# Performance work log

Measured on AMD Instinct MI355X. Metric: run time of the kernel, lower is better.

## Reference

```python
import jax, jax.numpy as jnp
import numpy as np

B, NPG, H, D = 16, 4096, 2, 64            # graphs, nodes/graph, heads, in_channels
N = B * NPG                                # 65536 total nodes
E_PER = 32768                              # edges per graph (avg degree 8)
E = B * E_PER                              # 524288 total edges
K_ORDER = 4
BETA = 0.5
D_OUT = 64


def setup_inputs():
    key = jax.random.key(0)
    k = jax.random.split(key, 10)
    x = jax.random.normal(k[0], (N, D), jnp.float32)
    # intra-graph random edges (block-diagonal adjacency)
    src = jax.random.randint(k[1], (B, E_PER), 0, NPG)
    dst = jax.random.randint(k[2], (B, E_PER), 0, NPG)
    off = (jnp.arange(B) * NPG)[:, None]
    edge_index = jnp.stack([(src + off).reshape(-1), (dst + off).reshape(-1)], axis=0)
    batch = jnp.arange(N) // NPG
    s = 1.0 / np.sqrt(D)
    Wq = jax.random.normal(k[3], (D, D * H), jnp.float32) * s
    bq = jnp.zeros((D * H,), jnp.float32)
    Wk = jax.random.normal(k[4], (D, D * H), jnp.float32) * s
    bk = jnp.zeros((D * H,), jnp.float32)
    Wo = jax.random.normal(k[5], (D * H, D_OUT), jnp.float32) * (1.0 / np.sqrt(D * H))
    bo = jnp.zeros((D_OUT,), jnp.float32)
    return {"x": x, "edge_index": edge_index, "batch": batch,
            "Wq": Wq, "bq": bq, "Wk": Wk, "bk": bk, "Wo": Wo, "bo": bo}


def reference(x, edge_index, batch, Wq, bq, Wk, bk, Wo, bo):
    Nn = x.shape[0]
    q = (x @ Wq + bq).reshape(Nn, H, D)
    k = (x @ Wk + bk).reshape(Nn, H, D)
    qs = q / jnp.linalg.norm(q, axis=2, keepdims=True)
    ks = k / jnp.linalg.norm(k, axis=2, keepdims=True)

    # symmetric-normalized transposed adjacency: adj_t[col_e, row_e] = w_e
    row, col = edge_index[0], edge_index[1]
    w = jnp.ones((row.shape[0],), x.dtype)
    deg = jax.ops.segment_sum(w, col, num_segments=N)
    dinv = jnp.where(deg > 0, deg ** -0.5, 0.0)
    val = dinv[col] * w * dinv[row]

    def gcn(xs):  # xs [N,H,D]; out[i] = sum_{e: col_e==i} val_e * xs[row_e]
        return jax.ops.segment_sum(val[:, None, None] * xs[row], col, num_segments=N)

    # ragged block <-> padded batch conversion (block-sorted batch ids)
    counts = jax.ops.segment_sum(jnp.ones((Nn,), jnp.int32), batch, num_segments=B)
    starts = jnp.concatenate([jnp.zeros((1,), jnp.int32), jnp.cumsum(counts)[:-1]])
    pos = jnp.arange(Nn) - starts[batch]

    def to_batch(v):
        return jnp.zeros((B, NPG) + v.shape[1:], v.dtype).at[batch, pos].set(v)

    def to_block(v):
        return v[batch, pos]

    qs_b, ks_b = to_batch(qs), to_batch(ks)      # [B, NPG, H, D]
    xs = jnp.broadcast_to(x[:, None, :], (Nn, H, D))
    xs_b = to_batch(xs)

    # linear (kernelized) attention; note source adds B (=qs.shape[0]) to the
    # denominator and uses the pre-loop xs_batch for every iteration -- kept faithful.
    kvs = jnp.einsum('blhm,blhd->bhmd', ks_b, xs_b)
    qkvs = jnp.einsum('bnhm,bhmd->bnhd', qs_b, kvs)
    num = qkvs + xs_b.sum(axis=1)[:, None]                       # [B,NPG,H,D]
    den = jnp.einsum('bnhm,bhm->bnh', qs_b, ks_b.sum(axis=1))[..., None] + float(B)
    attn_blk = to_block(num / den)                               # [N,H,D]

    for _ in range(K_ORDER):
        xs = xs + BETA * gcn(xs) + (1.0 - BETA) * attn_blk

    return (xs.reshape(Nn, H * D) @ Wo + bo) / H
```

## Files before the change

### kernel.cpp

```cpp
#include <hip/hip_runtime.h>

#define N_NODES 65536
#define B_G     16
#define NPG_    4096
#define H_H     2
#define D_D     64
#define HD      128
#define E_E     524288
#define D_OUT   64


__global__ void deg_kernel(const int* __restrict__ col, int* __restrict__ degi) {
    int e = blockIdx.x * 256 + threadIdx.x;
    if (e < E_E) atomicAdd(&degi[col[e]], 1);
}

__global__ void scan1(const int* __restrict__ degi, int* __restrict__ ptr,
                      int* __restrict__ bsums, float* __restrict__ dinv) {
    __shared__ int lds[256];
    int t = threadIdx.x;
    int i = blockIdx.x * 256 + t;
    int v = degi[i];
    dinv[i] = (v > 0) ? (1.0f / sqrtf((float)v)) : 0.0f;
    lds[t] = v;
    __syncthreads();
    for (int off = 1; off < 256; off <<= 1) {
        int tmp = (t >= off) ? lds[t - off] : 0;
        __syncthreads();
        lds[t] += tmp;
        __syncthreads();
    }
    ptr[i] = lds[t] - v;
    if (t == 255) bsums[blockIdx.x] = lds[255];
}

__global__ void scan3(int* __restrict__ ptr, const int* __restrict__ bsums) {
    __shared__ int red[256];
    int t = threadIdx.x;
    red[t] = (t < (int)blockIdx.x) ? bsums[t] : 0;
    __syncthreads();
    for (int off = 128; off > 0; off >>= 1) {
        if (t < off) red[t] += red[t + off];
        __syncthreads();
    }
    int i = blockIdx.x * 256 + t;
    ptr[i] += red[0];
    if (i == 0) ptr[N_NODES] = E_E;
}

__global__ void scatter_kernel(const int* __restrict__ row, const int* __restrict__ col,
                               const int* __restrict__ ptr, int* __restrict__ cursor,
                               const float* __restrict__ dinv,
                               int2* __restrict__ ep) {
    int e = blockIdx.x * 256 + threadIdx.x;
    if (e < E_E) {
        int c = col[e], r = row[e];
        int p = ptr[c] + atomicAdd(&cursor[c], 1);
        ep[p] = make_int2(r, __float_as_int(dinv[c] * dinv[r]));
    }
}

__global__ __launch_bounds__(256) void proj_kernel(
    const float* __restrict__ x,
    const float* __restrict__ Wq, const float* __restrict__ bq,
    const float* __restrict__ Wk, const float* __restrict__ bk,
    float* __restrict__ qs, float* __restrict__ ks) {
    __shared__ float4 wt4[16 * 128];
    __shared__ float4 xt4[64 * 17];
    __shared__ float bl[128];
    int t = threadIdx.x;
    int qk = blockIdx.x & 1;
    int nb = (blockIdx.x >> 1) * 64;
    const float* W = qk ? Wk : Wq;
    const float* bias = qk ? bk : bq;
    float* outp = qk ? ks : qs;

    for (int i = t; i < 2048; i += 256) {
        int k4 = i >> 7, c = i & 127;
        wt4[i] = make_float4(W[(4 * k4 + 0) * 128 + c], W[(4 * k4 + 1) * 128 + c],
                             W[(4 * k4 + 2) * 128 + c], W[(4 * k4 + 3) * 128 + c]);
    }
    const float4* xg = (const float4*)(x + (size_t)nb * 64);
    for (int i = t; i < 1024; i += 256) {
        int node = i >> 4, k4 = i & 15;
        xt4[node * 17 + k4] = xg[i];
    }
    if (t < 128) bl[t] = bias[t];
    __syncthreads();

    int cg = t & 15;
    int nd = (t >> 4) & 3;
    int w = t >> 6;
    int n_t = w * 16 + nd * 4;

    float acc[4][8];
#pragma unroll
    for (int i = 0; i < 4; ++i)
#pragma unroll
        for (int j = 0; j < 8; ++j) acc[i][j] = 0.f;

#pragma unroll 2
    for (int k4 = 0; k4 < 16; ++k4) {
        float4 xv0 = xt4[(n_t + 0) * 17 + k4];
        float4 xv1 = xt4[(n_t + 1) * 17 + k4];
        float4 xv2 = xt4[(n_t + 2) * 17 + k4];
        float4 xv3 = xt4[(n_t + 3) * 17 + k4];
#pragma unroll
        for (int j = 0; j < 8; ++j) {
            float4 wv = wt4[k4 * 128 + cg + 16 * j];
            acc[0][j] += wv.x * xv0.x + wv.y * xv0.y + wv.z * xv0.z + wv.w * xv0.w;
            acc[1][j] += wv.x * xv1.x + wv.y * xv1.y + wv.z * xv1.z + wv.w * xv1.w;
            acc[2][j] += wv.x * xv2.x + wv.y * xv2.y + wv.z * xv2.z + wv.w * xv2.w;
            acc[3][j] += wv.x * xv3.x + wv.y * xv3.y + wv.z * xv3.z + wv.w * xv3.w;
        }
    }

    float bcol[8];
#pragma unroll
    for (int j = 0; j < 8; ++j) bcol[j] = bl[cg + 16 * j];

#pragma unroll
    for (int i = 0; i < 4; ++i) {
#pragma unroll
        for (int j = 0; j < 8; ++j) acc[i][j] += bcol[j];
        float s0 = acc[i][0] * acc[i][0] + acc[i][1] * acc[i][1] +
                   acc[i][2] * acc[i][2] + acc[i][3] * acc[i][3];
        float s1 = acc[i][4] * acc[i][4] + acc[i][5] * acc[i][5] +
                   acc[i][6] * acc[i][6] + acc[i][7] * acc[i][7];
#pragma unroll
        for (int off = 8; off > 0; off >>= 1) {
            s0 += __shfl_xor(s0, off);
            s1 += __shfl_xor(s1, off);
        }
        float r0 = rsqrtf(s0), r1 = rsqrtf(s1);
        size_t base = (size_t)(nb + n_t + i) * 128 + cg;
#pragma unroll
        for (int j = 0; j < 4; ++j) outp[base + 16 * j] = acc[i][j] * r0;
#pragma unroll
        for (int j = 4; j < 8; ++j) outp[base + 16 * j] = acc[i][j] * r1;
    }
}

__global__ __launch_bounds__(256) void kvs_part(
    const float* __restrict__ ks, const float* __restrict__ x,
    float* __restrict__ partials, float* __restrict__ ksum, float* __restrict__ xsum) {
    int bid = blockIdx.x;
    int chunk = bid & 31;
    int bh = bid >> 5;
    int b = bh >> 1, h = bh & 1;
    int t = threadIdx.x;
    int mrow = t >> 4, dcol = t & 15;
    int m0 = mrow * 4, d0 = dcol * 4;
    __shared__ float kl[32 * 64];
    __shared__ float xl[32 * 64];
    float acc[4][4] = {{0}};
    float ksacc[4] = {0, 0, 0, 0};
    float xsacc[4] = {0, 0, 0, 0};
    int node0 = b * NPG_ + chunk * 128;
    for (int s = 0; s < 4; ++s) {
        int nb = node0 + s * 32;
        for (int i = t; i < 512; i += 256) {
            int l = i >> 4, q = i & 15;
            ((float4*)kl)[i] = *(const float4*)(ks + (size_t)(nb + l) * 128 + h * 64 + q * 4);
        }
        const float4* xg = (const float4*)(x + (size_t)nb * 64);
        for (int i = t; i < 512; i += 256) ((float4*)xl)[i] = xg[i];
        __syncthreads();
        for (int l = 0; l < 32; ++l) {
            float4 kv = *(float4*)(kl + l * 64 + m0);
            float4 xv = *(float4*)(xl + l * 64 + d0);
            float kk[4] = {kv.x, kv.y, kv.z, kv.w};
            float xx[4] = {xv.x, xv.y, xv.z, xv.w};
#pragma unroll
            for (int i = 0; i < 4; ++i)
#pragma unroll
                for (int j = 0; j < 4; ++j) acc[i][j] += kk[i] * xx[j];
            if (dcol == 0) {
#pragma unroll
                for (int i = 0; i < 4; ++i) ksacc[i] += kk[i];
            }
            if (mrow == 0) {
#pragma unroll
                for (int j = 0; j < 4; ++j) xsacc[j] += xx[j];
            }
        }
        __syncthreads();
    }
    float* pout = partials + (size_t)bid * 4096;
#pragma unroll
    for (int i = 0; i < 4; ++i)
        *(float4*)(pout + (m0 + i) * 64 + d0) =
            make_float4(acc[i][0], acc[i][1], acc[i][2], acc[i][3]);
    if (dcol == 0) {
#pragma unroll
        for (int i = 0; i < 4; ++i) atomicAdd(&ksum[bh * 64 + m0 + i], ksacc[i]);
    }
    if (mrow == 0 && h == 0) {
#pragma unroll
        for (int j = 0; j < 4; ++j) atomicAdd(&xsum[b * 64 + d0 + j], xsacc[j]);
    }
}

__global__ __launch_bounds__(256) void kvs_reduce(
    const float* __restrict__ partials, float* __restrict__ kvs) {
    int i = blockIdx.x * 256 + threadIdx.x;
    int bh = i >> 12, elem = i & 4095;
    const float* p = partials + (size_t)bh * 32 * 4096 + elem;
    float s = 0.f;
#pragma unroll
    for (int c = 0; c < 32; ++c) s += p[c * 4096];
    kvs[i] = s;
}

__global__ __launch_bounds__(256) void attn_kernel(
    const float* __restrict__ qs, const float* __restrict__ kvs,
    const float* __restrict__ ksum, const float* __restrict__ xsum,
    float* __restrict__ attn) {
    __shared__ float ql[128 * 64];
    int bid = blockIdx.x;
    int h = bid & 1;
    int nb = (bid >> 1) * 128;
    int b = nb >> 12;
    int bh = b * 2 + h;
    int t = threadIdx.x;
    int lane = t & 63;
    for (int i = t; i < 128 * 16; i += 256) {
        int r = i >> 4, q4 = i & 15;
        ((float4*)ql)[i] = *(const float4*)(qs + (size_t)(nb + r) * 128 + h * 64 + q4 * 4);
    }
    float kvreg[64];
    const float* kvp = kvs + bh * 4096 + lane;
#pragma unroll
    for (int m = 0; m < 64; ++m) kvreg[m] = kvp[m * 64];
    float ksreg = ksum[bh * 64 + lane];
    float xs_d = xsum[b * 64 + lane];
    __syncthreads();
    int nslot = t >> 6;
    for (int nn = 0; nn < 32; ++nn) {
        int node = nn * 4 + nslot;
        const float* qrow = ql + node * 64;
        float p = qrow[lane] * ksreg;
#pragma unroll
        for (int off = 32; off > 0; off >>= 1) p += __shfl_xor(p, off);
        float den = p + 16.0f;
        float acc = 0.f;
#pragma unroll
        for (int m4 = 0; m4 < 16; ++m4) {
            float4 qv = *(const float4*)(qrow + m4 * 4);
            acc += qv.x * kvreg[4 * m4] + qv.y * kvreg[4 * m4 + 1] +
                   qv.z * kvreg[4 * m4 + 2] + qv.w * kvreg[4 * m4 + 3];
        }
        attn[(size_t)(nb + node) * 128 + h * 64 + lane] = (acc + xs_d) / den;
    }
}

__global__ __launch_bounds__(256) void awo_kernel(
    const float* __restrict__ attn, const float* __restrict__ Wo,
    float* __restrict__ a) {
    __shared__ float4 wt4[32 * 64];
    __shared__ float4 xt4[64 * 32];
    int t = threadIdx.x;
    int nb = blockIdx.x * 64;

    for (int i = t; i < 2048; i += 256) {
        int k4 = i >> 6, c = i & 63;
        wt4[i] = make_float4(Wo[(4 * k4 + 0) * 64 + c], Wo[(4 * k4 + 1) * 64 + c],
                             Wo[(4 * k4 + 2) * 64 + c], Wo[(4 * k4 + 3) * 64 + c]);
    }
    const float4* ag = (const float4*)(attn + (size_t)nb * 128);
    for (int i = t; i < 2048; i += 256) xt4[i] = ag[i];
    __syncthreads();

    int cg = t & 15;
    int ns = t >> 4;
    int s = ns & 3;
    int n_t = ns * 4;

    float acc[4][4] = {{0.f}};
#pragma unroll 4
    for (int k4 = 0; k4 < 32; ++k4) {
        int kk = k4 ^ s;
        float4 xv0 = xt4[(n_t + 0) * 32 + kk];
        float4 xv1 = xt4[(n_t + 1) * 32 + kk];
        float4 xv2 = xt4[(n_t + 2) * 32 + kk];
        float4 xv3 = xt4[(n_t + 3) * 32 + kk];
#pragma unroll
        for (int j = 0; j < 4; ++j) {
            float4 wv = wt4[kk * 64 + cg + 16 * j];
            acc[0][j] += wv.x * xv0.x + wv.y * xv0.y + wv.z * xv0.z + wv.w * xv0.w;
            acc[1][j] += wv.x * xv1.x + wv.y * xv1.y + wv.z * xv1.z + wv.w * xv1.w;
            acc[2][j] += wv.x * xv2.x + wv.y * xv2.y + wv.z * xv2.z + wv.w * xv2.w;
            acc[3][j] += wv.x * xv3.x + wv.y * xv3.y + wv.z * xv3.z + wv.w * xv3.w;
        }
    }
#pragma unroll
    for (int i = 0; i < 4; ++i)
#pragma unroll
        for (int j = 0; j < 4; ++j)
            a[(size_t)(nb + n_t + i) * 64 + cg + 16 * j] = acc[i][j];
}

__global__ __launch_bounds__(256) void y0_kernel(
    const float* __restrict__ x, const float* __restrict__ Wo,
    float* __restrict__ y0) {
    __shared__ float4 wt4[16 * 64];
    __shared__ float4 xt4[64 * 16];
    int t = threadIdx.x;
    int nb = blockIdx.x * 64;

    for (int i = t; i < 1024; i += 256) {
        int k4 = i >> 6, c = i & 63;
        wt4[i] = make_float4(
            Wo[(4 * k4 + 0) * 64 + c] + Wo[(4 * k4 + 64) * 64 + c],
            Wo[(4 * k4 + 1) * 64 + c] + Wo[(4 * k4 + 65) * 64 + c],
            Wo[(4 * k4 + 2) * 64 + c] + Wo[(4 * k4 + 66) * 64 + c],
            Wo[(4 * k4 + 3) * 64 + c] + Wo[(4 * k4 + 67) * 64 + c]);
    }
    const float4* xg = (const float4*)(x + (size_t)nb * 64);
    for (int i = t; i < 1024; i += 256) xt4[i] = xg[i];
    __syncthreads();

    int cg = t & 15;
    int ns = t >> 4;
    int s = ns & 3;
    int n_t = ns * 4;

    float acc[4][4] = {{0.f}};
#pragma unroll 4
    for (int k4 = 0; k4 < 16; ++k4) {
        int kk = k4 ^ s;
        float4 xv0 = xt4[(n_t + 0) * 16 + kk];
        float4 xv1 = xt4[(n_t + 1) * 16 + kk];
        float4 xv2 = xt4[(n_t + 2) * 16 + kk];
        float4 xv3 = xt4[(n_t + 3) * 16 + kk];
#pragma unroll
        for (int j = 0; j < 4; ++j) {
            float4 wv = wt4[kk * 64 + cg + 16 * j];
            acc[0][j] += wv.x * xv0.x + wv.y * xv0.y + wv.z * xv0.z + wv.w * xv0.w;
            acc[1][j] += wv.x * xv1.x + wv.y * xv1.y + wv.z * xv1.z + wv.w * xv1.w;
            acc[2][j] += wv.x * xv2.x + wv.y * xv2.y + wv.z * xv2.z + wv.w * xv2.w;
            acc[3][j] += wv.x * xv3.x + wv.y * xv3.y + wv.z * xv3.z + wv.w * xv3.w;
        }
    }
#pragma unroll
    for (int i = 0; i < 4; ++i)
#pragma unroll
        for (int j = 0; j < 4; ++j)
            y0[(size_t)(nb + n_t + i) * 64 + cg + 16 * j] = acc[i][j];
}

template <int LAST>
__global__ __launch_bounds__(256) void gcn64_kernel(
    const float* __restrict__ yin, const float* __restrict__ a,
    const int* __restrict__ ptr, const int2* __restrict__ ep,
    float* __restrict__ yout, const float* __restrict__ bo) {
    int bid = blockIdx.x;
    int lbid = (bid & 7) * (N_NODES / 16 / 8) + (bid >> 3);
    int t = threadIdx.x;
    int n = lbid * 16 + (t >> 4);
    int lg = t & 15;
    int c4 = lg * 4;
    int e0 = ptr[n], e1 = ptr[n + 1];
    int cnt = e1 - e0;
    float4 acc = make_float4(0.f, 0.f, 0.f, 0.f);

    {
        int2 q[8];
#pragma unroll
        for (int i = 0; i < 8; ++i) {
            int ee = e0 + i;
            if (ee > e1 - 1) ee = e1 - 1;
            if (ee < 0) ee = 0;
            q[i] = ep[ee];
        }
#pragma unroll
        for (int i = 0; i < 8; ++i) {
            if (i < cnt) {
                float v = __int_as_float(q[i].y);
                float4 xv = *(const float4*)(yin + (size_t)q[i].x * 64 + c4);
                acc.x += v * xv.x; acc.y += v * xv.y;
                acc.z += v * xv.z; acc.w += v * xv.w;
            }
        }
    }
    if (cnt > 8) {
        int2 q[8];
#pragma unroll
        for (int i = 0; i < 8; ++i) {
            int ee = e0 + 8 + i;
            if (ee > e1 - 1) ee = e1 - 1;
            q[i] = ep[ee];
        }
#pragma unroll
        for (int i = 0; i < 8; ++i) {
            if (8 + i < cnt) {
                float v = __int_as_float(q[i].y);
                float4 xv = *(const float4*)(yin + (size_t)q[i].x * 64 + c4);
                acc.x += v * xv.x; acc.y += v * xv.y;
                acc.z += v * xv.z; acc.w += v * xv.w;
            }
        }
        for (int e = e0 + 16; e < e1; ++e) {
            int2 qq = ep[e];
            float v = __int_as_float(qq.y);
            float4 xv = *(const float4*)(yin + (size_t)qq.x * 64 + c4);
            acc.x += v * xv.x; acc.y += v * xv.y;
            acc.z += v * xv.z; acc.w += v * xv.w;
        }
    }

    size_t idx = (size_t)n * 64 + c4;
    float4 self = *(const float4*)(yin + idx);
    float4 at = *(const float4*)(a + idx);
    float4 o;
    o.x = self.x + 0.5f * acc.x + 0.5f * at.x;
    o.y = self.y + 0.5f * acc.y + 0.5f * at.y;
    o.z = self.z + 0.5f * acc.z + 0.5f * at.z;
    o.w = self.w + 0.5f * acc.w + 0.5f * at.w;
    if (LAST) {
        float4 bv = *(const float4*)(bo + c4);
        o.x = (o.x + bv.x) * 0.5f;
        o.y = (o.y + bv.y) * 0.5f;
        o.z = (o.z + bv.z) * 0.5f;
        o.w = (o.w + bv.w) * 0.5f;
    }
    *(float4*)(yout + idx) = o;
}


extern "C" void kernel_launch(void* const* d_in, const int* in_sizes, int n_in,
                              void* d_out, int out_size, void* d_ws, size_t ws_size,
                              hipStream_t stream) {
    const float* x  = (const float*)d_in[0];
    const int* ei   = (const int*)d_in[1];
    const float* Wq = (const float*)d_in[3];
    const float* bq = (const float*)d_in[4];
    const float* Wk = (const float*)d_in[5];
    const float* bk = (const float*)d_in[6];
    const float* Wo = (const float*)d_in[7];
    const float* bo = (const float*)d_in[8];
    float* out = (float*)d_out;

    const int* row = ei;
    const int* col = ei + E_E;

    float* bufA = (float*)d_ws;
    float* bufB = bufA + (size_t)N_NODES * HD;
    float* bufC = bufB + (size_t)N_NODES * HD;
    int2*  ep   = (int2*)(bufC + (size_t)N_NODES * HD);
    float* kvs  = (float*)(ep + E_E);
    float* ksum = kvs + 131072;
    float* xsum = ksum + 2048;
    float* dinv = xsum + 1024;
    int* degi   = (int*)(dinv + N_NODES);
    int* cursor = degi + N_NODES;
    int* ptr    = cursor + N_NODES;
    int* bsums  = ptr + N_NODES + 1;

    float* a_  = bufA;
    float* yA  = bufA + (size_t)N_NODES * 64;
    float* yB  = bufB;

    hipMemsetAsync(degi, 0, (size_t)N_NODES * 2 * 4, stream);
    hipMemsetAsync(ksum, 0, (size_t)(2048 + 1024) * 4, stream);

    deg_kernel<<<E_E / 256, 256, 0, stream>>>(col, degi);
    scan1<<<N_NODES / 256, 256, 0, stream>>>(degi, ptr, bsums, dinv);
    scan3<<<N_NODES / 256, 256, 0, stream>>>(ptr, bsums);
    scatter_kernel<<<E_E / 256, 256, 0, stream>>>(row, col, ptr, cursor, dinv, ep);

    proj_kernel<<<2048, 256, 0, stream>>>(x, Wq, bq, Wk, bk, bufA, bufB);

    kvs_part<<<1024, 256, 0, stream>>>(bufB, x, bufC, ksum, xsum);
    kvs_reduce<<<512, 256, 0, stream>>>(bufC, kvs);
    attn_kernel<<<1024, 256, 0, stream>>>(bufA, kvs, ksum, xsum, bufC);

    awo_kernel<<<1024, 256, 0, stream>>>(bufC, Wo, a_);
    y0_kernel<<<1024, 256, 0, stream>>>(x, Wo, yA);

    gcn64_kernel<0><<<N_NODES / 16, 256, 0, stream>>>(yA, a_, ptr, ep, yB, bo);
    gcn64_kernel<0><<<N_NODES / 16, 256, 0, stream>>>(yB, a_, ptr, ep, yA, bo);
    gcn64_kernel<0><<<N_NODES / 16, 256, 0, stream>>>(yA, a_, ptr, ep, yB, bo);
    gcn64_kernel<1><<<N_NODES / 16, 256, 0, stream>>>(yB, a_, ptr, ep, out, bo);
}
```

Measured before the change: 357.6 us.

## Retile projection and attention as register-blocked GEMMs, flatten GCN edge prefetch

The projection kernel now handles 128 nodes per block with an 8x8 register tile and XOR-swizzled shared memory in place of padding. The grid is halved to match. The attention kernel is rewritten from a per-lane 64-register kvs dot product into a tiled GEMM that stages kvs transposed in shared memory and computes the denominator inside the same loop. The GCN kernel unconditionally prefetches 16 edge entries instead of two conditional batches of 8. These changes aim for more register reuse and fewer bank conflicts, at the cost of more registers per thread and more redundant edge loads for low-degree nodes.

```diff
diff --git a/kernel.cpp b/kernel.cpp
--- a/kernel.cpp
+++ b/kernel.cpp
@@ -60,17 +60,16 @@
     }
 }
 
-__global__ __launch_bounds__(256) void proj_kernel(
+__global__ __launch_bounds__(256, 2) void proj_kernel(
     const float* __restrict__ x,
     const float* __restrict__ Wq, const float* __restrict__ bq,
     const float* __restrict__ Wk, const float* __restrict__ bk,
     float* __restrict__ qs, float* __restrict__ ks) {
     __shared__ float4 wt4[16 * 128];
-    __shared__ float4 xt4[64 * 17];
-    __shared__ float bl[128];
+    __shared__ float4 xt4[128 * 16];
     int t = threadIdx.x;
     int qk = blockIdx.x & 1;
-    int nb = (blockIdx.x >> 1) * 64;
+    int nb = (blockIdx.x >> 1) * 128;
     const float* W = qk ? Wk : Wq;
     const float* bias = qk ? bk : bq;
     float* outp = qk ? ks : qs;
@@ -81,46 +80,43 @@
                              W[(4 * k4 + 2) * 128 + c], W[(4 * k4 + 3) * 128 + c]);
     }
     const float4* xg = (const float4*)(x + (size_t)nb * 64);
-    for (int i = t; i < 1024; i += 256) {
+    for (int i = t; i < 2048; i += 256) {
         int node = i >> 4, k4 = i & 15;
-        xt4[node * 17 + k4] = xg[i];
-    }
-    if (t < 128) bl[t] = bias[t];
+        xt4[node * 16 + (k4 ^ (node & 7))] = xg[i];
+    }
     __syncthreads();
 
     int cg = t & 15;
-    int nd = (t >> 4) & 3;
-    int w = t >> 6;
-    int n_t = w * 16 + nd * 4;
-
-    float acc[4][8];
-#pragma unroll
-    for (int i = 0; i < 4; ++i)
+    int ns = t >> 4;
+    int sw = ns & 7;
+
+    float acc[8][8];
+#pragma unroll
+    for (int i = 0; i < 8; ++i)
 #pragma unroll
         for (int j = 0; j < 8; ++j) acc[i][j] = 0.f;
 
-#pragma unroll 2
     for (int k4 = 0; k4 < 16; ++k4) {
-        float4 xv0 = xt4[(n_t + 0) * 17 + k4];
-        float4 xv1 = xt4[(n_t + 1) * 17 + k4];
-        float4 xv2 = xt4[(n_t + 2) * 17 + k4];
-        float4 xv3 = xt4[(n_t + 3) * 17 + k4];
-#pragma unroll
-        for (int j = 0; j < 8; ++j) {
-            float4 wv = wt4[k4 * 128 + cg + 16 * j];
-            acc[0][j] += wv.x * xv0.x + wv.y * xv0.y + wv.z * xv0.z + wv.w * xv0.w;
-            acc[1][j] += wv.x * xv1.x + wv.y * xv1.y + wv.z * xv1.z + wv.w * xv1.w;
-            acc[2][j] += wv.x * xv2.x + wv.y * xv2.y + wv.z * xv2.z + wv.w * xv2.w;
-            acc[3][j] += wv.x * xv3.x + wv.y * xv3.y + wv.z * xv3.z + wv.w * xv3.w;
+        float4 wv[8];
+#pragma unroll
+        for (int j = 0; j < 8; ++j) wv[j] = wt4[k4 * 128 + cg + 16 * j];
+        int kx = k4 ^ sw;
+#pragma unroll
+        for (int i = 0; i < 8; ++i) {
+            float4 xv = xt4[(ns + 16 * i) * 16 + kx];
+#pragma unroll
+            for (int j = 0; j < 8; ++j)
+                acc[i][j] += wv[j].x * xv.x + wv[j].y * xv.y +
+                             wv[j].z * xv.z + wv[j].w * xv.w;
         }
     }
 
     float bcol[8];
 #pragma unroll
-    for (int j = 0; j < 8; ++j) bcol[j] = bl[cg + 16 * j];
-
-#pragma unroll
-    for (int i = 0; i < 4; ++i) {
+    for (int j = 0; j < 8; ++j) bcol[j] = bias[cg + 16 * j];
+
+#pragma unroll
+    for (int i = 0; i < 8; ++i) {
 #pragma unroll
         for (int j = 0; j < 8; ++j) acc[i][j] += bcol[j];
         float s0 = acc[i][0] * acc[i][0] + acc[i][1] * acc[i][1] +
@@ -133,7 +129,7 @@
             s1 += __shfl_xor(s1, off);
         }
         float r0 = rsqrtf(s0), r1 = rsqrtf(s1);
-        size_t base = (size_t)(nb + n_t + i) * 128 + cg;
+        size_t base = (size_t)(nb + ns + 16 * i) * 128 + cg;
 #pragma unroll
         for (int j = 0; j < 4; ++j) outp[base + 16 * j] = acc[i][j] * r0;
 #pragma unroll
@@ -212,45 +208,77 @@
     kvs[i] = s;
 }
 
-__global__ __launch_bounds__(256) void attn_kernel(
+__global__ __launch_bounds__(256, 3) void attn_kernel(
     const float* __restrict__ qs, const float* __restrict__ kvs,
     const float* __restrict__ ksum, const float* __restrict__ xsum,
     float* __restrict__ attn) {
-    __shared__ float ql[128 * 64];
+    __shared__ float4 wt4[16 * 64];
+    __shared__ float4 xt4[128 * 16];
+    __shared__ float4 ksv[16];
+    __shared__ float xsv[64];
     int bid = blockIdx.x;
     int h = bid & 1;
     int nb = (bid >> 1) * 128;
     int b = nb >> 12;
     int bh = b * 2 + h;
     int t = threadIdx.x;
-    int lane = t & 63;
-    for (int i = t; i < 128 * 16; i += 256) {
-        int r = i >> 4, q4 = i & 15;
-        ((float4*)ql)[i] = *(const float4*)(qs + (size_t)(nb + r) * 128 + h * 64 + q4 * 4);
-    }
-    float kvreg[64];
-    const float* kvp = kvs + bh * 4096 + lane;
-#pragma unroll
-    for (int m = 0; m < 64; ++m) kvreg[m] = kvp[m * 64];
-    float ksreg = ksum[bh * 64 + lane];
-    float xs_d = xsum[b * 64 + lane];
-    __syncthreads();
-    int nslot = t >> 6;
-    for (int nn = 0; nn < 32; ++nn) {
-        int node = nn * 4 + nslot;
-        const float* qrow = ql + node * 64;
-        float p = qrow[lane] * ksreg;
-#pragma unroll
-        for (int off = 32; off > 0; off >>= 1) p += __shfl_xor(p, off);
-        float den = p + 16.0f;
-        float acc = 0.f;
-#pragma unroll
-        for (int m4 = 0; m4 < 16; ++m4) {
-            float4 qv = *(const float4*)(qrow + m4 * 4);
-            acc += qv.x * kvreg[4 * m4] + qv.y * kvreg[4 * m4 + 1] +
-                   qv.z * kvreg[4 * m4 + 2] + qv.w * kvreg[4 * m4 + 3];
-        }
-        attn[(size_t)(nb + node) * 128 + h * 64 + lane] = (acc + xs_d) / den;
+
+    const float* kvp = kvs + (size_t)bh * 4096;
+    for (int i = t; i < 1024; i += 256) {
+        int k4 = i >> 6, d = i & 63;
+        wt4[i] = make_float4(kvp[(4 * k4 + 0) * 64 + d], kvp[(4 * k4 + 1) * 64 + d],
+                             kvp[(4 * k4 + 2) * 64 + d], kvp[(4 * k4 + 3) * 64 + d]);
+    }
+    for (int i = t; i < 2048; i += 256) {
+        int node = i >> 4, k4 = i & 15;
+        xt4[node * 16 + (k4 ^ (node & 7))] =
+            *(const float4*)(qs + (size_t)(nb + node) * 128 + h * 64 + 4 * k4);
+    }
+    if (t < 16) ksv[t] = *(const float4*)(ksum + bh * 64 + 4 * t);
+    if (t < 64) xsv[t] = xsum[b * 64 + t];
+    __syncthreads();
+
+    int cg = t & 15;
+    int ns = t >> 4;
+    int sw = ns & 7;
+
+    float acc[8][4];
+    float den[8];
+#pragma unroll
+    for (int i = 0; i < 8; ++i) {
+        den[i] = 0.f;
+#pragma unroll
+        for (int j = 0; j < 4; ++j) acc[i][j] = 0.f;
+    }
+
+    for (int k4 = 0; k4 < 16; ++k4) {
+        float4 kv = ksv[k4];
+        float4 wv[4];
+#pragma unroll
+        for (int j = 0; j < 4; ++j) wv[j] = wt4[k4 * 64 + cg + 16 * j];
+        int kx = k4 ^ sw;
+#pragma unroll
+        for (int i = 0; i < 8; ++i) {
+            float4 xv = xt4[(ns + 16 * i) * 16 + kx];
+            den[i] += kv.x * xv.x + kv.y * xv.y + kv.z * xv.z + kv.w * xv.w;
+#pragma unroll
+            for (int j = 0; j < 4; ++j)
+                acc[i][j] += wv[j].x * xv.x + wv[j].y * xv.y +
+                             wv[j].z * xv.z + wv[j].w * xv.w;
+        }
+    }
+
+    float xs_d[4];
+#pragma unroll
+    for (int j = 0; j < 4; ++j) xs_d[j] = xsv[cg + 16 * j];
+
+#pragma unroll
+    for (int i = 0; i < 8; ++i) {
+        float inv = 1.0f / (den[i] + 16.0f);
+        size_t base = (size_t)(nb + ns + 16 * i) * 128 + h * 64 + cg;
+#pragma unroll
+        for (int j = 0; j < 4; ++j)
+            attn[base + 16 * j] = (acc[i][j] + xs_d[j]) * inv;
     }
 }
 
@@ -364,49 +392,29 @@
     int cnt = e1 - e0;
     float4 acc = make_float4(0.f, 0.f, 0.f, 0.f);
 
-    {
-        int2 q[8];
-#pragma unroll
-        for (int i = 0; i < 8; ++i) {
-            int ee = e0 + i;
-            if (ee > e1 - 1) ee = e1 - 1;
-            if (ee < 0) ee = 0;
-            q[i] = ep[ee];
-        }
-#pragma unroll
-        for (int i = 0; i < 8; ++i) {
-            if (i < cnt) {
-                float v = __int_as_float(q[i].y);
-                float4 xv = *(const float4*)(yin + (size_t)q[i].x * 64 + c4);
-                acc.x += v * xv.x; acc.y += v * xv.y;
-                acc.z += v * xv.z; acc.w += v * xv.w;
-            }
-        }
-    }
-    if (cnt > 8) {
-        int2 q[8];
-#pragma unroll
-        for (int i = 0; i < 8; ++i) {
-            int ee = e0 + 8 + i;
-            if (ee > e1 - 1) ee = e1 - 1;
-            q[i] = ep[ee];
-        }
-#pragma unroll
-        for (int i = 0; i < 8; ++i) {
-            if (8 + i < cnt) {
-                float v = __int_as_float(q[i].y);
-                float4 xv = *(const float4*)(yin + (size_t)q[i].x * 64 + c4);
-                acc.x += v * xv.x; acc.y += v * xv.y;
-                acc.z += v * xv.z; acc.w += v * xv.w;
-            }
-        }
-        for (int e = e0 + 16; e < e1; ++e) {
-            int2 qq = ep[e];
-            float v = __int_as_float(qq.y);
-            float4 xv = *(const float4*)(yin + (size_t)qq.x * 64 + c4);
+    int2 q[16];
+#pragma unroll
+    for (int i = 0; i < 16; ++i) {
+        int ee = e0 + i;
+        if (ee > e1 - 1) ee = e1 - 1;
+        if (ee < 0) ee = 0;
+        q[i] = ep[ee];
+    }
+#pragma unroll
+    for (int i = 0; i < 16; ++i) {
+        if (i < cnt) {
+            float v = __int_as_float(q[i].y);
+            float4 xv = *(const float4*)(yin + (size_t)q[i].x * 64 + c4);
             acc.x += v * xv.x; acc.y += v * xv.y;
             acc.z += v * xv.z; acc.w += v * xv.w;
         }
+    }
+    for (int e = e0 + 16; e < e1; ++e) {
+        int2 qq = ep[e];
+        float v = __int_as_float(qq.y);
+        float4 xv = *(const float4*)(yin + (size_t)qq.x * 64 + c4);
+        acc.x += v * xv.x; acc.y += v * xv.y;
+        acc.z += v * xv.z; acc.w += v * xv.w;
     }
 
     size_t idx = (size_t)n * 64 + c4;
@@ -469,7 +477,7 @@
     scan3<<<N_NODES / 256, 256, 0, stream>>>(ptr, bsums);
     scatter_kernel<<<E_E / 256, 256, 0, stream>>>(row, col, ptr, cursor, dinv, ep);
 
-    proj_kernel<<<2048, 256, 0, stream>>>(x, Wq, bq, Wk, bk, bufA, bufB);
+    proj_kernel<<<1024, 256, 0, stream>>>(x, Wq, bq, Wk, bk, bufA, bufB);
 
     kvs_part<<<1024, 256, 0, stream>>>(bufB, x, bufC, ksum, xsum);
     kvs_reduce<<<512, 256, 0, stream>>>(bufC, kvs);
```

Measured after the change: 359.7 us. About the same (+0.6%).
